# Kernel tuning notes

Measured on AMD Instinct MI355X. Metric: run time of the kernel, lower is better.

The kernel has to match this reference:

```python
import jax, jax.numpy as jnp
import numpy as np
import math

B, T = 64, 2000
RNN_DIM, EMB_DIM, ATT_DIM = 1024, 512, 128
STATIC_CH, STATIC_K = 8, 21
DYN_CH, DYN_K = 8, 21
PRIOR_LEN, ALPHA, BETA = 11, 0.1, 0.9


def _betabinom_pmf(k, n, a, b):
    lg = math.lgamma
    return math.exp(lg(n + 1) - lg(k + 1) - lg(n - k + 1)
                    + lg(k + a) + lg(n - k + b) - lg(n + a + b)
                    - (lg(a) + lg(b) - lg(a + b)))


def setup_inputs() -> dict:
    key = jax.random.key(0)
    ks = jax.random.split(key, 12)
    query = jax.random.normal(ks[0], (B, RNN_DIM), jnp.float32)
    memory = jax.random.normal(ks[1], (B, T, EMB_DIM), jnp.float32)
    a = jax.random.uniform(ks[2], (B, T), jnp.float32)
    alignment_pre = a / jnp.sum(a, axis=1, keepdims=True)  # valid attention distribution
    mask = jnp.zeros((B, T), dtype=bool)
    s = 1.0 / math.sqrt(RNN_DIM)
    W_w = jax.random.uniform(ks[3], (ATT_DIM, RNN_DIM), jnp.float32, -s, s)
    W_b = jax.random.uniform(ks[4], (ATT_DIM,), jnp.float32, -s, s)
    V_w = jax.random.normal(ks[5], (DYN_CH * DYN_K, ATT_DIM), jnp.float32) * 0.05
    F_w = jax.random.normal(ks[6], (STATIC_CH, 1, STATIC_K), jnp.float32) * 0.1
    U_w = jax.random.normal(ks[7], (ATT_DIM, STATIC_CH), jnp.float32) * 0.1
    T_w = jax.random.normal(ks[8], (ATT_DIM, DYN_CH), jnp.float32) * 0.1
    T_b = jax.random.normal(ks[9], (ATT_DIM,), jnp.float32) * 0.05
    v_w = jax.random.normal(ks[10], (1, ATT_DIM), jnp.float32) * 0.1
    P_np = np.array([_betabinom_pmf(k, PRIOR_LEN - 1, ALPHA, BETA) for k in range(PRIOR_LEN)], np.float32)
    P = jnp.asarray(P_np[::-1].copy())  # buffer: flipped beta-binomial prior
    return {"attention_hidden_state": query, "memory": memory, "alignment_pre": alignment_pre,
            "mask": mask, "W_w": W_w, "W_b": W_b, "V_w": V_w, "F_w": F_w,
            "U_w": U_w, "T_w": T_w, "T_b": T_b, "v_w": v_w, "P": P}


def _conv1d(lhs, rhs, pad, groups=1):
    # lhs [N,C,T], rhs [O,C//groups,K]; cross-correlation, matching torch conv1d
    return jax.lax.conv_general_dilated(lhs, rhs, (1,), [pad],
                                        dimension_numbers=("NCH", "OIH", "NCH"),
                                        feature_group_count=groups)


def reference(attention_hidden_state, memory, alignment_pre, mask,
              W_w, W_b, V_w, F_w, U_w, T_w, T_b, v_w, P):
    b, t = alignment_pre.shape
    # log of causal beta-binomial prior: left-pad by prior_length-1, valid conv
    p = _conv1d(alignment_pre[:, None, :], P.reshape(1, 1, -1), (PRIOR_LEN - 1, 0))[:, 0, :]
    p = jnp.log(jnp.clip(p, 1e-6))
    # per-sample dynamic kernels: [B, dyn_ch*K]
    G = jnp.tanh(attention_hidden_state @ W_w.T + W_b) @ V_w.T
    g = _conv1d(alignment_pre[None, :, :], G.reshape(b * DYN_CH, 1, DYN_K),
                ((DYN_K - 1) // 2, (DYN_K - 1) // 2), groups=b)  # [1, B*dyn_ch, T]
    g = g.reshape(b, DYN_CH, t).transpose(0, 2, 1)  # [B, T, dyn_ch]
    # static conv features
    f = _conv1d(alignment_pre[:, None, :], F_w,
                ((STATIC_K - 1) // 2, (STATIC_K - 1) // 2)).transpose(0, 2, 1)  # [B, T, static_ch]
    e = (jnp.tanh(f @ U_w.T + g @ T_w.T + T_b) @ v_w.T)[..., 0] + p  # [B, T]
    e = jnp.where(mask, -jnp.inf, e)
    attention_weights = jax.nn.softmax(e, axis=1)
    attention_context = jnp.einsum("bt,bte->be", attention_weights, memory)
    return attention_context, attention_weights
```

## Files before the change

### kernel.cpp

```cpp
#include <hip/hip_runtime.h>

#define B_   64
#define T_   2000
#define RNN_ 1024
#define EMB_ 512
#define ATT_ 128
#define CH_  8
#define K_   21
#define PL_  11
#define GSZ  168
#define ECHK 256
#define NEC  8
#define CCHK 64
#define NCC  32

typedef float vf4 __attribute__((ext_vector_type(4)));

__device__ __forceinline__ float fast_tanh(float x) {
    float ax = fabsf(x);
    float e  = __expf(2.0f * ax);
    float t  = 1.0f - 2.0f / (e + 1.0f);
    return copysignf(t, x);
}

__global__ __launch_bounds__(256) void k_gen_dyn(
    const float* __restrict__ q, const float* __restrict__ Ww,
    const float* __restrict__ Wb, const float* __restrict__ Vw,
    float* __restrict__ G)
{
    __shared__ float sq[RNN_];
    __shared__ float part[256];
    __shared__ float sh[ATT_];
    const int b = blockIdx.x, tid = threadIdx.x;
    for (int i = tid; i < RNN_; i += 256) sq[i] = q[b * RNN_ + i];
    __syncthreads();
    {
        const int row = tid & 127, half = tid >> 7;
        const float4* wr = reinterpret_cast<const float4*>(Ww + row * RNN_ + half * (RNN_ / 2));
        const float4* qr = reinterpret_cast<const float4*>(sq + half * (RNN_ / 2));
        float acc = 0.f;
        #pragma unroll 8
        for (int i = 0; i < RNN_ / 8; ++i) {
            float4 w4 = wr[i], q4 = qr[i];
            acc += w4.x * q4.x + w4.y * q4.y + w4.z * q4.z + w4.w * q4.w;
        }
        part[tid] = acc;
    }
    __syncthreads();
    if (tid < ATT_) sh[tid] = fast_tanh(part[tid] + part[tid + 128] + Wb[tid]);
    __syncthreads();
    for (int o = tid; o < GSZ; o += 256) {
        const float4* vr = reinterpret_cast<const float4*>(Vw + o * ATT_);
        const float4* hr = reinterpret_cast<const float4*>(sh);
        float acc = 0.f;
        #pragma unroll 8
        for (int i = 0; i < ATT_ / 4; ++i) {
            float4 v4 = vr[i], h4 = hr[i];
            acc += v4.x * h4.x + v4.y * h4.y + v4.z * h4.z + v4.w * h4.w;
        }
        G[b * GSZ + o] = acc;
    }
}

__global__ __launch_bounds__(256) void k_energy(
    const float* __restrict__ a,  const float* __restrict__ G,
    const float* __restrict__ Fw, const float* __restrict__ Uw,
    const float* __restrict__ Tw, const float* __restrict__ Tb,
    const float* __restrict__ vw, const float* __restrict__ P,
    const unsigned char* __restrict__ mask,
    float* __restrict__ pout, float* __restrict__ mred, float* __restrict__ sred)
{
    __shared__ float sA[ECHK + K_ - 1];
    __shared__ float sFG[K_ * 16];
    __shared__ float sUT[ATT_ * 16];
    __shared__ float sTb[ATT_], sV[ATT_], sPr[PL_];
    __shared__ float red[4];
    const int b = blockIdx.x, chunk = blockIdx.y, tid = threadIdx.x;
    const int t0 = chunk * ECHK;
    const int base = t0 - (K_ - 1) / 2;

    for (int j = tid; j < ECHK + K_ - 1; j += 256) {
        int idx = base + j;
        sA[j] = (idx >= 0 && idx < T_) ? a[b * T_ + idx] : 0.f;
    }
    for (int j = tid; j < 2 * GSZ; j += 256) {
        if (j < GSZ) sFG[(j % K_) * 16 + (j / K_)] = Fw[j];
        else { int jj = j - GSZ; sFG[(jj % K_) * 16 + 8 + (jj / K_)] = G[b * GSZ + jj]; }
    }
    for (int j = tid; j < ATT_ * CH_; j += 256) {
        int d = j >> 3, c = j & 7;
        sUT[d * 16 + c]     = Uw[j];
        sUT[d * 16 + 8 + c] = Tw[j];
    }
    if (tid < ATT_) { sTb[tid] = Tb[tid]; sV[tid] = vw[tid]; }
    if (tid < PL_)  sPr[tid] = P[tid];
    __syncthreads();

    const int t = t0 + tid;
    const bool valid = (t < T_) && !mask[b * T_ + min(t, T_ - 1)];

    float fg[16];
    #pragma unroll
    for (int i = 0; i < 16; ++i) fg[i] = 0.f;
    #pragma unroll
    for (int k = 0; k < K_; ++k) {
        float av = sA[tid + k];
        const float4* fp = reinterpret_cast<const float4*>(&sFG[k * 16]);
        float4 x0 = fp[0], x1 = fp[1], x2 = fp[2], x3 = fp[3];
        fg[0]  += x0.x * av; fg[1]  += x0.y * av; fg[2]  += x0.z * av; fg[3]  += x0.w * av;
        fg[4]  += x1.x * av; fg[5]  += x1.y * av; fg[6]  += x1.z * av; fg[7]  += x1.w * av;
        fg[8]  += x2.x * av; fg[9]  += x2.y * av; fg[10] += x2.z * av; fg[11] += x2.w * av;
        fg[12] += x3.x * av; fg[13] += x3.y * av; fg[14] += x3.z * av; fg[15] += x3.w * av;
    }
    float pp = 0.f;
    #pragma unroll
    for (int k = 0; k < PL_; ++k) pp += sPr[k] * sA[tid + k];

    float acc = 0.f;
    #pragma unroll 4
    for (int d = 0; d < ATT_; ++d) {
        const float4* up = reinterpret_cast<const float4*>(&sUT[d * 16]);
        float4 u0 = up[0], u1 = up[1], u2 = up[2], u3 = up[3];
        float s = sTb[d];
        s += u0.x * fg[0]  + u0.y * fg[1]  + u0.z * fg[2]  + u0.w * fg[3];
        s += u1.x * fg[4]  + u1.y * fg[5]  + u1.z * fg[6]  + u1.w * fg[7];
        s += u2.x * fg[8]  + u2.y * fg[9]  + u2.z * fg[10] + u2.w * fg[11];
        s += u3.x * fg[12] + u3.y * fg[13] + u3.z * fg[14] + u3.w * fg[15];
        acc += sV[d] * fast_tanh(s);
    }
    float e = valid ? (acc + __logf(fmaxf(pp, 1e-6f))) : -1e30f;

    float m = e;
    #pragma unroll
    for (int off = 32; off > 0; off >>= 1) m = fmaxf(m, __shfl_xor(m, off));
    if ((tid & 63) == 0) red[tid >> 6] = m;
    __syncthreads();
    const float Mc = fmaxf(fmaxf(red[0], red[1]), fmaxf(red[2], red[3]));
    __syncthreads();
    float pv = valid ? __expf(e - Mc) : 0.f;
    if (t < T_) pout[b * T_ + t] = pv;
    float ssum = pv;
    #pragma unroll
    for (int off = 32; off > 0; off >>= 1) ssum += __shfl_xor(ssum, off);
    if ((tid & 63) == 0) red[tid >> 6] = ssum;
    __syncthreads();
    if (tid == 0) {
        mred[b * NEC + chunk] = Mc;
        sred[b * NEC + chunk] = red[0] + red[1] + red[2] + red[3];
    }
}

__global__ __launch_bounds__(256) void k_ctx(
    const float* __restrict__ mred, const float* __restrict__ sred,
    const float* __restrict__ mem, float* __restrict__ w,
    float* __restrict__ out)
{
    __shared__ float sw[CCHK];
    __shared__ vf4 sCtx[2][EMB_ / 4];
    const int b = blockIdx.x, chunk = blockIdx.y, tid = threadIdx.x;
    const int t0 = chunk * CCHK;
    const int nvalid = min(CCHK, T_ - t0);

    float mv[NEC], sv[NEC];
    {
        const float4* mp = reinterpret_cast<const float4*>(mred + b * NEC);
        const float4* sp = reinterpret_cast<const float4*>(sred + b * NEC);
        float4 m0 = mp[0], m1 = mp[1], s0 = sp[0], s1 = sp[1];
        mv[0]=m0.x; mv[1]=m0.y; mv[2]=m0.z; mv[3]=m0.w;
        mv[4]=m1.x; mv[5]=m1.y; mv[6]=m1.z; mv[7]=m1.w;
        sv[0]=s0.x; sv[1]=s0.y; sv[2]=s0.z; sv[3]=s0.w;
        sv[4]=s1.x; sv[5]=s1.y; sv[6]=s1.z; sv[7]=s1.w;
    }
    float M = mv[0];
    #pragma unroll
    for (int i = 1; i < NEC; ++i) M = fmaxf(M, mv[i]);
    float S = 0.f;
    #pragma unroll
    for (int i = 0; i < NEC; ++i) S += sv[i] * __expf(mv[i] - M);
    const float scale = __expf(mv[chunk >> 2] - M) / S;

    if (tid < CCHK) {
        const int t = t0 + tid;
        float wv = 0.f;
        if (t < T_) {
            wv = w[b * T_ + t] * scale;
            w[b * T_ + t] = wv;
        }
        sw[tid] = wv;
    }
    __syncthreads();

    const int col = tid & 127, rp = tid >> 7;
    const vf4* m4 = reinterpret_cast<const vf4*>(mem + ((size_t)(b * T_ + t0)) * EMB_);
    vf4 acc = {0.f, 0.f, 0.f, 0.f};
    if (nvalid == CCHK) {
        #pragma unroll 8
        for (int tt = rp; tt < CCHK; tt += 2) {
            float wv = sw[tt];
            vf4 mvv = __builtin_nontemporal_load(m4 + (size_t)tt * (EMB_ / 4) + col);
            acc += wv * mvv;
        }
    } else {
        for (int tt = rp; tt < nvalid; tt += 2) {
            float wv = sw[tt];
            vf4 mvv = __builtin_nontemporal_load(m4 + (size_t)tt * (EMB_ / 4) + col);
            acc += wv * mvv;
        }
    }
    sCtx[rp][col] = acc;
    __syncthreads();
    if (tid < EMB_ / 4) {
        vf4 r = sCtx[0][tid];
        r += sCtx[1][tid];
        float* op = out + b * EMB_ + tid * 4;
        atomicAdd(op + 0, r.x); atomicAdd(op + 1, r.y);
        atomicAdd(op + 2, r.z); atomicAdd(op + 3, r.w);
    }
}

extern "C" void kernel_launch(void* const* d_in, const int* in_sizes, int n_in,
                              void* d_out, int out_size, void* d_ws, size_t ws_size,
                              hipStream_t stream)
{
    const float* q    = (const float*)d_in[0];
    const float* mem  = (const float*)d_in[1];
    const float* a    = (const float*)d_in[2];
    const unsigned char* mask = (const unsigned char*)d_in[3];
    const float* Ww = (const float*)d_in[4];
    const float* Wb = (const float*)d_in[5];
    const float* Vw = (const float*)d_in[6];
    const float* Fw = (const float*)d_in[7];
    const float* Uw = (const float*)d_in[8];
    const float* Tw = (const float*)d_in[9];
    const float* Tb = (const float*)d_in[10];
    const float* vw = (const float*)d_in[11];
    const float* P  = (const float*)d_in[12];

    float* out_ctx = (float*)d_out;
    float* out_w   = out_ctx + B_ * EMB_;

    float* G    = (float*)d_ws;
    float* mred = G + B_ * GSZ;
    float* sred = mred + B_ * NEC;

    hipMemsetAsync(out_ctx, 0, B_ * EMB_ * sizeof(float), stream);
    k_gen_dyn<<<B_, 256, 0, stream>>>(q, Ww, Wb, Vw, G);
    k_energy<<<dim3(B_, NEC), 256, 0, stream>>>(a, G, Fw, Uw, Tw, Tb, vw, P,
                                                mask, out_w, mred, sred);
    k_ctx<<<dim3(B_, NCC), 256, 0, stream>>>(mred, sred, mem, out_w, out_ctx);
}
```

Measured before the change: 99.66 us.

## Split energy ATT reduction across two thread halves and fold memset into gen kernel

The energy kernel now covers 128 timesteps per block, with two thread halves each computing 64 of the 128 attention dimensions. Their partial sums are combined through shared memory, which doubles the block count and halves the serial tanh loop per thread. The output memset is folded into the dynamic-kernel generator to save a launch. The context kernel gets a launch-bounds occupancy hint, reads 16 chunk partials, and switches from nontemporal to regular loads. The trade-off is duplicated conv work per half and an extra barrier.

```diff
diff --git a/kernel.cpp b/kernel.cpp
--- a/kernel.cpp
+++ b/kernel.cpp
@@ -9,8 +9,8 @@
 #define K_   21
 #define PL_  11
 #define GSZ  168
-#define ECHK 256
-#define NEC  8
+#define ECHK 128
+#define NEC  16
 #define CCHK 64
 #define NCC  32
 
@@ -26,12 +26,13 @@
 __global__ __launch_bounds__(256) void k_gen_dyn(
     const float* __restrict__ q, const float* __restrict__ Ww,
     const float* __restrict__ Wb, const float* __restrict__ Vw,
-    float* __restrict__ G)
+    float* __restrict__ G, float* __restrict__ out_ctx)
 {
     __shared__ float sq[RNN_];
     __shared__ float part[256];
     __shared__ float sh[ATT_];
     const int b = blockIdx.x, tid = threadIdx.x;
+    for (int i = tid; i < EMB_; i += 256) out_ctx[b * EMB_ + i] = 0.f;
     for (int i = tid; i < RNN_; i += 256) sq[i] = q[b * RNN_ + i];
     __syncthreads();
     {
@@ -74,10 +75,13 @@
     __shared__ float sFG[K_ * 16];
     __shared__ float sUT[ATT_ * 16];
     __shared__ float sTb[ATT_], sV[ATT_], sPr[PL_];
+    __shared__ float sQ[2 * ECHK];
     __shared__ float red[4];
     const int b = blockIdx.x, chunk = blockIdx.y, tid = threadIdx.x;
     const int t0 = chunk * ECHK;
     const int base = t0 - (K_ - 1) / 2;
+    const int tloc = tid & (ECHK - 1);
+    const int h = tid >> 7;
 
     for (int j = tid; j < ECHK + K_ - 1; j += 256) {
         int idx = base + j;
@@ -96,15 +100,12 @@
     if (tid < PL_)  sPr[tid] = P[tid];
     __syncthreads();
 
-    const int t = t0 + tid;
-    const bool valid = (t < T_) && !mask[b * T_ + min(t, T_ - 1)];
-
     float fg[16];
     #pragma unroll
     for (int i = 0; i < 16; ++i) fg[i] = 0.f;
     #pragma unroll
     for (int k = 0; k < K_; ++k) {
-        float av = sA[tid + k];
+        float av = sA[tloc + k];
         const float4* fp = reinterpret_cast<const float4*>(&sFG[k * 16]);
         float4 x0 = fp[0], x1 = fp[1], x2 = fp[2], x3 = fp[3];
         fg[0]  += x0.x * av; fg[1]  += x0.y * av; fg[2]  += x0.z * av; fg[3]  += x0.w * av;
@@ -112,24 +113,35 @@
         fg[8]  += x2.x * av; fg[9]  += x2.y * av; fg[10] += x2.z * av; fg[11] += x2.w * av;
         fg[12] += x3.x * av; fg[13] += x3.y * av; fg[14] += x3.z * av; fg[15] += x3.w * av;
     }
-    float pp = 0.f;
-    #pragma unroll
-    for (int k = 0; k < PL_; ++k) pp += sPr[k] * sA[tid + k];
-
-    float acc = 0.f;
+
+    float accQ = 0.f;
+    const int d0 = h * 64;
     #pragma unroll 4
-    for (int d = 0; d < ATT_; ++d) {
+    for (int dd = 0; dd < 64; ++dd) {
+        const int d = d0 + dd;
         const float4* up = reinterpret_cast<const float4*>(&sUT[d * 16]);
         float4 u0 = up[0], u1 = up[1], u2 = up[2], u3 = up[3];
-        float s = sTb[d];
-        s += u0.x * fg[0]  + u0.y * fg[1]  + u0.z * fg[2]  + u0.w * fg[3];
-        s += u1.x * fg[4]  + u1.y * fg[5]  + u1.z * fg[6]  + u1.w * fg[7];
-        s += u2.x * fg[8]  + u2.y * fg[9]  + u2.z * fg[10] + u2.w * fg[11];
-        s += u3.x * fg[12] + u3.y * fg[13] + u3.z * fg[14] + u3.w * fg[15];
-        acc += sV[d] * fast_tanh(s);
-    }
-    float e = valid ? (acc + __logf(fmaxf(pp, 1e-6f))) : -1e30f;
-
+        float s0 = u0.x * fg[0]  + u0.y * fg[1]  + u0.z * fg[2]  + u0.w * fg[3];
+        float s1 = u1.x * fg[4]  + u1.y * fg[5]  + u1.z * fg[6]  + u1.w * fg[7];
+        float s2 = u2.x * fg[8]  + u2.y * fg[9]  + u2.z * fg[10] + u2.w * fg[11];
+        float s3 = u3.x * fg[12] + u3.y * fg[13] + u3.z * fg[14] + u3.w * fg[15];
+        float s = (sTb[d] + s0) + (s1 + s2) + s3;
+        accQ += sV[d] * fast_tanh(s);
+    }
+    sQ[h * ECHK + tloc] = accQ;
+    __syncthreads();
+
+    float e = -1e30f;
+    const int t = t0 + tid;
+    if (tid < ECHK) {
+        const bool valid = (t < T_) && !mask[b * T_ + min(t, T_ - 1)];
+        if (valid) {
+            float pp = 0.f;
+            #pragma unroll
+            for (int k = 0; k < PL_; ++k) pp += sPr[k] * sA[tid + k];
+            e = sQ[tid] + sQ[ECHK + tid] + __logf(fmaxf(pp, 1e-6f));
+        }
+    }
     float m = e;
     #pragma unroll
     for (int off = 32; off > 0; off >>= 1) m = fmaxf(m, __shfl_xor(m, off));
@@ -137,8 +149,8 @@
     __syncthreads();
     const float Mc = fmaxf(fmaxf(red[0], red[1]), fmaxf(red[2], red[3]));
     __syncthreads();
-    float pv = valid ? __expf(e - Mc) : 0.f;
-    if (t < T_) pout[b * T_ + t] = pv;
+    float pv = (e > -1e29f) ? __expf(e - Mc) : 0.f;
+    if (tid < ECHK && t < T_) pout[b * T_ + t] = pv;
     float ssum = pv;
     #pragma unroll
     for (int off = 32; off > 0; off >>= 1) ssum += __shfl_xor(ssum, off);
@@ -150,34 +162,34 @@
     }
 }
 
-__global__ __launch_bounds__(256) void k_ctx(
+__global__ __launch_bounds__(256, 8) void k_ctx(
     const float* __restrict__ mred, const float* __restrict__ sred,
     const float* __restrict__ mem, float* __restrict__ w,
     float* __restrict__ out)
 {
-    __shared__ float sw[CCHK];
+    __shared__ float sw_[CCHK];
     __shared__ vf4 sCtx[2][EMB_ / 4];
     const int b = blockIdx.x, chunk = blockIdx.y, tid = threadIdx.x;
     const int t0 = chunk * CCHK;
     const int nvalid = min(CCHK, T_ - t0);
 
-    float mv[NEC], sv[NEC];
-    {
-        const float4* mp = reinterpret_cast<const float4*>(mred + b * NEC);
-        const float4* sp = reinterpret_cast<const float4*>(sred + b * NEC);
-        float4 m0 = mp[0], m1 = mp[1], s0 = sp[0], s1 = sp[1];
-        mv[0]=m0.x; mv[1]=m0.y; mv[2]=m0.z; mv[3]=m0.w;
-        mv[4]=m1.x; mv[5]=m1.y; mv[6]=m1.z; mv[7]=m1.w;
-        sv[0]=s0.x; sv[1]=s0.y; sv[2]=s0.z; sv[3]=s0.w;
-        sv[4]=s1.x; sv[5]=s1.y; sv[6]=s1.z; sv[7]=s1.w;
-    }
-    float M = mv[0];
-    #pragma unroll
-    for (int i = 1; i < NEC; ++i) M = fmaxf(M, mv[i]);
-    float S = 0.f;
-    #pragma unroll
-    for (int i = 0; i < NEC; ++i) S += sv[i] * __expf(mv[i] - M);
-    const float scale = __expf(mv[chunk >> 2] - M) / S;
+    const float4* mp = reinterpret_cast<const float4*>(mred + b * NEC);
+    const float4* sp = reinterpret_cast<const float4*>(sred + b * NEC);
+    float4 m0 = mp[0], m1 = mp[1], m2 = mp[2], m3 = mp[3];
+    float M = fmaxf(fmaxf(fmaxf(m0.x, m0.y), fmaxf(m0.z, m0.w)),
+             fmaxf(fmaxf(fmaxf(m1.x, m1.y), fmaxf(m1.z, m1.w)),
+             fmaxf(fmaxf(fmaxf(m2.x, m2.y), fmaxf(m2.z, m2.w)),
+                   fmaxf(fmaxf(m3.x, m3.y), fmaxf(m3.z, m3.w)))));
+    float4 s0 = sp[0], s1 = sp[1], s2 = sp[2], s3 = sp[3];
+    float S = s0.x * __expf(m0.x - M) + s0.y * __expf(m0.y - M)
+            + s0.z * __expf(m0.z - M) + s0.w * __expf(m0.w - M)
+            + s1.x * __expf(m1.x - M) + s1.y * __expf(m1.y - M)
+            + s1.z * __expf(m1.z - M) + s1.w * __expf(m1.w - M)
+            + s2.x * __expf(m2.x - M) + s2.y * __expf(m2.y - M)
+            + s2.z * __expf(m2.z - M) + s2.w * __expf(m2.w - M)
+            + s3.x * __expf(m3.x - M) + s3.y * __expf(m3.y - M)
+            + s3.z * __expf(m3.z - M) + s3.w * __expf(m3.w - M);
+    const float scale = __expf(mred[b * NEC + (chunk >> 1)] - M) / S;
 
     if (tid < CCHK) {
         const int t = t0 + tid;
@@ -186,7 +198,7 @@
             wv = w[b * T_ + t] * scale;
             w[b * T_ + t] = wv;
         }
-        sw[tid] = wv;
+        sw_[tid] = wv;
     }
     __syncthreads();
 
@@ -196,14 +208,14 @@
     if (nvalid == CCHK) {
         #pragma unroll 8
         for (int tt = rp; tt < CCHK; tt += 2) {
-            float wv = sw[tt];
-            vf4 mvv = __builtin_nontemporal_load(m4 + (size_t)tt * (EMB_ / 4) + col);
+            float wv = sw_[tt];
+            vf4 mvv = m4[(size_t)tt * (EMB_ / 4) + col];
             acc += wv * mvv;
         }
     } else {
         for (int tt = rp; tt < nvalid; tt += 2) {
-            float wv = sw[tt];
-            vf4 mvv = __builtin_nontemporal_load(m4 + (size_t)tt * (EMB_ / 4) + col);
+            float wv = sw_[tt];
+            vf4 mvv = m4[(size_t)tt * (EMB_ / 4) + col];
             acc += wv * mvv;
         }
     }
@@ -243,8 +255,7 @@
     float* mred = G + B_ * GSZ;
     float* sred = mred + B_ * NEC;
 
-    hipMemsetAsync(out_ctx, 0, B_ * EMB_ * sizeof(float), stream);
-    k_gen_dyn<<<B_, 256, 0, stream>>>(q, Ww, Wb, Vw, G);
+    k_gen_dyn<<<B_, 256, 0, stream>>>(q, Ww, Wb, Vw, G, out_ctx);
     k_energy<<<dim3(B_, NEC), 256, 0, stream>>>(a, G, Fw, Uw, Tw, Tb, vw, P,
                                                 mask, out_w, mred, sred);
     k_ctx<<<dim3(B_, NCC), 256, 0, stream>>>(mred, sred, mem, out_w, out_ctx);
```

New measurement: 94.22 us. 1.06x faster.
